# Kernel optimization log

Hardware: AMD Instinct MI355X
Metric: run time of the kernel (lower is better)

## Reference

```python
import jax, jax.numpy as jnp
import numpy as np
from jax import lax

FS = 48000.0
PI = 3.14159265358979323846

def bilinear_low_shelf(fc, gain_db, Q, fs):
    A = 10.0 ** (gain_db / 40.0)
    w0 = 2.0 * PI * fc / fs
    alpha = jnp.sin(w0) / (2.0 * Q)
    cosw = jnp.cos(w0)
    sqA = jnp.sqrt(A)
    b0 = A * (A + 1 - (A - 1) * cosw + 2 * sqA * alpha)
    b1 = 2 * A * (A - 1 - (A + 1) * cosw)
    b2 = A * (A + 1 - (A - 1) * cosw - 2 * sqA * alpha)
    a0 = A + 1 + (A - 1) * cosw + 2 * sqA * alpha
    a1 = -2 * (A - 1 + (A + 1) * cosw)
    a2 = A + 1 + (A - 1) * cosw - 2 * sqA * alpha
    return (b0 / a0, b1 / a0, b2 / a0, a1 / a0, a2 / a0)

def biquad(x, b0, b1, b2, a1, a2):
    # x: [B, T]; direct-form-II-transposed biquad with zero initial state
    B = x.shape[0]
    z0 = (jnp.zeros((B,), x.dtype), jnp.zeros((B,), x.dtype))
    def step(carry, xn):
        z1, z2 = carry
        yn = b0 * xn + z1
        z1n = b1 * xn - a1 * yn + z2
        z2n = b2 * xn - a2 * yn
        return (z1n, z2n), yn
    _, yT = lax.scan(step, z0, x.T)  # scan over time axis
    return yT.T

def setup_inputs() -> dict:
    key = jax.random.key(0)
    x = jax.random.normal(key, (64, 480000), dtype=jnp.float32)
    return {
        "x": x,
        "low_gain_db": jnp.float32(6.0),
        "mid_gain_db": jnp.float32(-3.0),
        "mid_fc": jnp.float32(800.0),
        "mid_Q": jnp.float32(1.0),
        "high_gain_db": jnp.float32(4.0),
    }

def reference(x, low_gain_db, mid_gain_db, mid_fc, mid_Q, high_gain_db):
    c = bilinear_low_shelf(jnp.float32(120.0), low_gain_db, jnp.float32(0.707), FS)
    y = biquad(x, *c)
    c = bilinear_low_shelf(mid_fc, mid_gain_db, mid_Q, FS)
    y = biquad(y, *c)
    c = bilinear_low_shelf(jnp.float32(4000.0), high_gain_db, jnp.float32(0.707), FS)
    y = biquad(y, *c)
    return y
```

## Files before the change

### kernel.cpp

```cpp
#include <hip/hip_runtime.h>
#include <math.h>


constexpr int T_LEN  = 480000;
constexpr int B_ROWS = 64;
constexpr int CHUNK  = 64;
constexpr int LOG2C  = 6;
constexpr int KCH    = T_LEN / CHUNK;
constexpr int NT     = 256;
constexpr int HISTC  = 24;
constexpr int MTERM  = 24;
constexpr int OUTC   = NT - HISTC;
constexpr int BLKROW = (KCH + OUTC - 1) / OUTC;
constexpr int NBLK   = B_ROWS * BLKROW;

struct Coeffs { float b0, b1, b2, a1, a2; };

__device__ __forceinline__ float rfl(float v) {
    return __int_as_float(__builtin_amdgcn_readfirstlane(__float_as_int(v)));
}

__device__ __forceinline__ Coeffs shelf(float fc, float gdb, float Q) {
    float A  = powf(10.0f, gdb * (1.0f / 40.0f));
    float w0 = 2.0f * 3.14159265358979323846f * fc / 48000.0f;
    float sw = sinf(w0), cw = cosf(w0);
    float alpha = sw / (2.0f * Q);
    float sqA = sqrtf(A);
    float b0 = A * ((A + 1.0f) - (A - 1.0f) * cw + 2.0f * sqA * alpha);
    float b1 = 2.0f * A * ((A - 1.0f) - (A + 1.0f) * cw);
    float b2 = A * ((A + 1.0f) - (A - 1.0f) * cw - 2.0f * sqA * alpha);
    float a0 = (A + 1.0f) + (A - 1.0f) * cw + 2.0f * sqA * alpha;
    float a1 = -2.0f * ((A - 1.0f) + (A + 1.0f) * cw);
    float a2 = (A + 1.0f) + (A - 1.0f) * cw - 2.0f * sqA * alpha;
    float rr = 1.0f / a0;
    Coeffs c;
    c.b0 = rfl(b0 * rr); c.b1 = rfl(b1 * rr); c.b2 = rfl(b2 * rr);
    c.a1 = rfl(a1 * rr); c.a2 = rfl(a2 * rr);
    return c;
}

__device__ __forceinline__ float bq(float xn, const Coeffs& c, float& z1, float& z2) {
    float y = fmaf(c.b0, xn, z1);
    z1 = fmaf(-c.a1, y, fmaf(c.b1, xn, z2));
    z2 = fmaf(c.b2, xn, -(c.a2 * y));
    return y;
}

__device__ __forceinline__ float step6(float s[6], float x,
                                       const Coeffs& c1, const Coeffs& c2, const Coeffs& c3) {
    float y1 = bq(x,  c1, s[0], s[1]);
    float y2 = bq(y1, c2, s[2], s[3]);
    float y3 = bq(y2, c3, s[4], s[5]);
    return y3;
}

__global__ __launch_bounds__(256, 4) void k_fused(
    const float* __restrict__ x,
    const float* __restrict__ p_lg, const float* __restrict__ p_mg,
    const float* __restrict__ p_mf, const float* __restrict__ p_mq,
    const float* __restrict__ p_hg,
    float* __restrict__ out)
{
    __shared__ float dl[NT * 7];
    __shared__ float M[36];

    const int t = threadIdx.x;
    const int r = blockIdx.x / BLKROW;
    const int b = blockIdx.x - r * BLKROW;
    const int c = b * OUTC + t - HISTC;
    const bool active = (c >= 0) && (c < KCH);
    const bool emit   = (t >= HISTC) && (c < KCH);

    Coeffs c1 = shelf(120.0f,  *p_lg, 0.707f);
    Coeffs c2 = shelf(*p_mf,   *p_mg, *p_mq);
    Coeffs c3 = shelf(4000.0f, *p_hg, 0.707f);

    float4 xv[16];
    {
        int cc = c < 0 ? 0 : c;
        const float4* lp = (const float4*)(x + (long long)r * T_LEN + (long long)cc * CHUNK);
        if (active) {
            #pragma unroll
            for (int q = 0; q < 16; ++q) xv[q] = lp[q];
        } else {
            #pragma unroll
            for (int q = 0; q < 16; ++q) xv[q] = make_float4(0.f, 0.f, 0.f, 0.f);
        }
    }

    float s[6] = {0.f, 0.f, 0.f, 0.f, 0.f, 0.f};
    #pragma unroll
    for (int q = 0; q < 16; ++q) {
        step6(s, xv[q].x, c1, c2, c3);
        step6(s, xv[q].y, c1, c2, c3);
        step6(s, xv[q].z, c1, c2, c3);
        step6(s, xv[q].w, c1, c2, c3);
    }
    #pragma unroll
    for (int i = 0; i < 6; ++i) dl[t * 7 + i] = s[i];

    if (t < 6) {
        float e[6] = {0.f, 0.f, 0.f, 0.f, 0.f, 0.f};
        e[t] = 1.0f;
        step6(e, 0.0f, c1, c2, c3);
        #pragma unroll
        for (int i = 0; i < 6; ++i) M[i * 6 + t] = e[i];
    }
    __syncthreads();
    for (int it = 0; it < LOG2C; ++it) {
        float acc = 0.f;
        if (t < 36) {
            int i = t / 6, j = t - 6 * (t / 6);
            #pragma unroll
            for (int q = 0; q < 6; ++q) acc = fmaf(M[i * 6 + q], M[q * 6 + j], acc);
        }
        __syncthreads();
        if (t < 36) M[t] = acc;
        __syncthreads();
    }
    float a[36];
    #pragma unroll
    for (int i = 0; i < 36; ++i) a[i] = rfl(M[i]);

    float t6[6] = {0.f, 0.f, 0.f, 0.f, 0.f, 0.f};
    int m0 = t - MTERM; if (m0 < 0) m0 = 0;
    for (int m = m0; m < t; ++m) {
        float dm[6];
        #pragma unroll
        for (int i = 0; i < 6; ++i) dm[i] = dl[m * 7 + i];
        float nt6[6];
        #pragma unroll
        for (int i = 0; i < 6; ++i) {
            float acc = dm[i];
            #pragma unroll
            for (int j = 0; j < 6; ++j) acc = fmaf(a[i * 6 + j], t6[j], acc);
            nt6[i] = acc;
        }
        #pragma unroll
        for (int i = 0; i < 6; ++i) t6[i] = nt6[i];
    }

    #pragma unroll
    for (int q = 0; q < 16; ++q) {
        float4 v = xv[q];
        v.x = step6(t6, v.x, c1, c2, c3);
        v.y = step6(t6, v.y, c1, c2, c3);
        v.z = step6(t6, v.z, c1, c2, c3);
        v.w = step6(t6, v.w, c1, c2, c3);
        xv[q] = v;
    }

    if (emit) {
        float4* sp = (float4*)(out + (long long)r * T_LEN + (long long)c * CHUNK);
        #pragma unroll
        for (int q = 0; q < 16; ++q) sp[q] = xv[q];
    }
}

extern "C" void kernel_launch(void* const* d_in, const int* in_sizes, int n_in,
                              void* d_out, int out_size, void* d_ws, size_t ws_size,
                              hipStream_t stream) {
    const float* x  = (const float*)d_in[0];
    const float* lg = (const float*)d_in[1];
    const float* mg = (const float*)d_in[2];
    const float* mf = (const float*)d_in[3];
    const float* mq = (const float*)d_in[4];
    const float* hg = (const float*)d_in[5];
    float* out = (float*)d_out;

    hipLaunchKernelGGL(k_fused, dim3(NBLK), dim3(NT), 0, stream,
                       x, lg, mg, mf, mq, hg, out);
}
```

Measured before the change: 251.4 us.

## Stage input via direct global-to-LDS loads with swizzle, coalesce output stores

Result: no change. 246.8 us (-1.8%).

```diff
diff --git a/kernel.cpp b/kernel.cpp
--- a/kernel.cpp
+++ b/kernel.cpp
@@ -13,8 +13,16 @@
 constexpr int OUTC   = NT - HISTC;
 constexpr int BLKROW = (KCH + OUTC - 1) / OUTC;
 constexpr int NBLK   = B_ROWS * BLKROW;
+constexpr long long XBYTES = (long long)B_ROWS * T_LEN * 4;
 
 struct Coeffs { float b0, b1, b2, a1, a2; };
+
+typedef __attribute__((address_space(1))) const void GV;
+typedef __attribute__((address_space(3))) void LV;
+
+__device__ __forceinline__ void gload_lds16(const void* g, void* l) {
+    __builtin_amdgcn_global_load_lds((GV*)g, (LV*)l, 16, 0, 0);
+}
 
 __device__ __forceinline__ float rfl(float v) {
     return __int_as_float(__builtin_amdgcn_readfirstlane(__float_as_int(v)));
@@ -54,73 +62,87 @@
     return y3;
 }
 
-__global__ __launch_bounds__(256, 4) void k_fused(
+__global__ __launch_bounds__(256, 2) void k_fused(
     const float* __restrict__ x,
     const float* __restrict__ p_lg, const float* __restrict__ p_mg,
     const float* __restrict__ p_mf, const float* __restrict__ p_mq,
     const float* __restrict__ p_hg,
     float* __restrict__ out)
 {
-    __shared__ float dl[NT * 7];
-    __shared__ float M[36];
-
-    const int t = threadIdx.x;
+    __shared__ __align__(16) float smem[16384 + NT * 7];
+
+    const int t    = threadIdx.x;
+    const int lane = t & 63;
+    const int w    = t >> 6;
     const int r = blockIdx.x / BLKROW;
     const int b = blockIdx.x - r * BLKROW;
     const int c = b * OUTC + t - HISTC;
+    const int cbase = b * OUTC - HISTC;
     const bool active = (c >= 0) && (c < KCH);
-    const bool emit   = (t >= HISTC) && (c < KCH);
 
     Coeffs c1 = shelf(120.0f,  *p_lg, 0.707f);
     Coeffs c2 = shelf(*p_mf,   *p_mg, *p_mq);
     Coeffs c3 = shelf(4000.0f, *p_hg, 0.707f);
-
-    float4 xv[16];
+    __builtin_amdgcn_sched_barrier(0);
+
+    float* svw = smem + w * 4096;
     {
-        int cc = c < 0 ? 0 : c;
-        const float4* lp = (const float4*)(x + (long long)r * T_LEN + (long long)cc * CHUNK);
-        if (active) {
+        long long wbyte = ((long long)r * T_LEN + (long long)(cbase + w * 64) * CHUNK) * 4;
+        #pragma unroll
+        for (int k = 0; k < 16; ++k) {
+            int d = k * 1024 + lane * 16;
+            int srel = d ^ (((d >> 8) & 7) << 4);
+            long long g = wbyte + srel;
+            g = g < 0 ? 0 : (g > XBYTES - 16 ? XBYTES - 16 : g);
+            gload_lds16((const char*)x + g, (char*)svw + k * 1024);
+        }
+    }
+
+    float a[36];
+    {
+        const int i = lane / 6;
+        const int j = lane - 6 * i;
+        float e[6];
+        #pragma unroll
+        for (int jj = 0; jj < 6; ++jj) e[jj] = (j == jj) ? 1.0f : 0.0f;
+        step6(e, 0.0f, c1, c2, c3);
+        float aM = e[0];
+        #pragma unroll
+        for (int ii = 1; ii < 6; ++ii) aM = (i == ii) ? e[ii] : aM;
+        const int i6 = i * 6;
+        for (int it = 0; it < LOG2C; ++it) {
+            float acc = 0.f;
             #pragma unroll
-            for (int q = 0; q < 16; ++q) xv[q] = lp[q];
-        } else {
-            #pragma unroll
-            for (int q = 0; q < 16; ++q) xv[q] = make_float4(0.f, 0.f, 0.f, 0.f);
-        }
-    }
-
+            for (int q = 0; q < 6; ++q) {
+                int sA = i6 + q; if (sA > 63) sA = 63;
+                float lhs = __shfl(aM, sA, 64);
+                float rhs = __shfl(aM, q * 6 + j, 64);
+                acc = fmaf(lhs, rhs, acc);
+            }
+            aM = acc;
+        }
+        #pragma unroll
+        for (int k = 0; k < 36; ++k) a[k] = rfl(__shfl(aM, k, 64));
+    }
+
+    asm volatile("s_waitcnt vmcnt(0)" ::: "memory");
+    __builtin_amdgcn_sched_barrier(0);
+    const int sb = lane * 16;
+    const int sx = lane & 7;
+    const float4* sv4 = (const float4*)svw;
     float s[6] = {0.f, 0.f, 0.f, 0.f, 0.f, 0.f};
     #pragma unroll
     for (int q = 0; q < 16; ++q) {
-        step6(s, xv[q].x, c1, c2, c3);
-        step6(s, xv[q].y, c1, c2, c3);
-        step6(s, xv[q].z, c1, c2, c3);
-        step6(s, xv[q].w, c1, c2, c3);
-    }
-    #pragma unroll
-    for (int i = 0; i < 6; ++i) dl[t * 7 + i] = s[i];
-
-    if (t < 6) {
-        float e[6] = {0.f, 0.f, 0.f, 0.f, 0.f, 0.f};
-        e[t] = 1.0f;
-        step6(e, 0.0f, c1, c2, c3);
-        #pragma unroll
-        for (int i = 0; i < 6; ++i) M[i * 6 + t] = e[i];
-    }
+        float4 v = sv4[sb + (q ^ sx)];
+        step6(s, v.x, c1, c2, c3);
+        step6(s, v.y, c1, c2, c3);
+        step6(s, v.z, c1, c2, c3);
+        step6(s, v.w, c1, c2, c3);
+    }
+    float* dl = smem + 16384;
+    #pragma unroll
+    for (int i = 0; i < 6; ++i) dl[t * 7 + i] = active ? s[i] : 0.f;
     __syncthreads();
-    for (int it = 0; it < LOG2C; ++it) {
-        float acc = 0.f;
-        if (t < 36) {
-            int i = t / 6, j = t - 6 * (t / 6);
-            #pragma unroll
-            for (int q = 0; q < 6; ++q) acc = fmaf(M[i * 6 + q], M[q * 6 + j], acc);
-        }
-        __syncthreads();
-        if (t < 36) M[t] = acc;
-        __syncthreads();
-    }
-    float a[36];
-    #pragma unroll
-    for (int i = 0; i < 36; ++i) a[i] = rfl(M[i]);
 
     float t6[6] = {0.f, 0.f, 0.f, 0.f, 0.f, 0.f};
     int m0 = t - MTERM; if (m0 < 0) m0 = 0;
@@ -133,27 +155,38 @@
         for (int i = 0; i < 6; ++i) {
             float acc = dm[i];
             #pragma unroll
-            for (int j = 0; j < 6; ++j) acc = fmaf(a[i * 6 + j], t6[j], acc);
+            for (int jj = 0; jj < 6; ++jj) acc = fmaf(a[i * 6 + jj], t6[jj], acc);
             nt6[i] = acc;
         }
         #pragma unroll
         for (int i = 0; i < 6; ++i) t6[i] = nt6[i];
     }
 
+    float4* svw4 = (float4*)svw;
     #pragma unroll
     for (int q = 0; q < 16; ++q) {
-        float4 v = xv[q];
+        int idx = sb + (q ^ sx);
+        float4 v = svw4[idx];
         v.x = step6(t6, v.x, c1, c2, c3);
         v.y = step6(t6, v.y, c1, c2, c3);
         v.z = step6(t6, v.z, c1, c2, c3);
         v.w = step6(t6, v.w, c1, c2, c3);
-        xv[q] = v;
-    }
-
-    if (emit) {
-        float4* sp = (float4*)(out + (long long)r * T_LEN + (long long)c * CHUNK);
-        #pragma unroll
-        for (int q = 0; q < 16; ++q) sp[q] = xv[q];
+        svw4[idx] = v;
+    }
+    asm volatile("s_waitcnt lgkmcnt(0)" ::: "memory");
+    __builtin_amdgcn_sched_barrier(0);
+
+    float4* op = (float4*)(out + (long long)r * T_LEN);
+    const long long f4base = (long long)(cbase + w * 64) * 16;
+    #pragma unroll
+    for (int jj = 0; jj < 16; ++jj) {
+        int o4 = jj * 64 + lane;
+        int so = o4 >> 4;
+        int tr = w * 64 + so;
+        int cc = cbase + tr;
+        if (tr >= HISTC && cc < KCH) {
+            op[f4base + o4] = svw4[o4 ^ (so & 7)];
+        }
     }
 }
 
```
